# Performance work log

Hardware: AMD Instinct MI355X
Metric: run time of the kernel (lower is better)

Reference implementation:

```python
import jax, jax.numpy as jnp
import numpy as np

B, L, D, M, H = 32, 4096, 512, 64, 8
HD = D // H  # head dim = 64
NEG = -1e9


def setup_inputs() -> dict:
    key = jax.random.key(0)
    ks = jax.random.split(key, 12)
    s = 1.0 / np.sqrt(D)
    return {
        "query_features": jax.random.normal(ks[0], (B, L, D), jnp.float32),
        "mask": jax.random.randint(ks[1], (B, L), 0, 2, jnp.int32),
        "memory": jax.random.normal(ks[2], (M, D), jnp.float32),
        "Wq": jax.random.normal(ks[3], (D, D), jnp.float32) * s,
        "bq": jax.random.normal(ks[4], (D,), jnp.float32) * 0.01,
        "Wk": jax.random.normal(ks[5], (D, D), jnp.float32) * s,
        "bk": jax.random.normal(ks[6], (D,), jnp.float32) * 0.01,
        "Wv": jax.random.normal(ks[7], (D, D), jnp.float32) * s,
        "bv": jax.random.normal(ks[8], (D,), jnp.float32) * 0.01,
        "Wo": jax.random.normal(ks[9], (D, D), jnp.float32) * s,
        "bo": jax.random.normal(ks[10], (D,), jnp.float32) * 0.01,
    }


def reference(query_features, mask, memory, Wq, bq, Wk, bk, Wv, bv, Wo, bo):
    # read_memory: MHA(query=features, key=value=memory broadcast over batch)
    # with additive attn_mask of -1e9 on rows whose query position is invalid
    # (torch masks every key for an invalid query -> uniform attention there).
    q = (query_features @ Wq.T + bq).reshape(B, L, H, HD)
    k = (memory @ Wk.T + bk).reshape(M, H, HD)   # shared across batch
    v = (memory @ Wv.T + bv).reshape(M, H, HD)
    scores = jnp.einsum('blhd,mhd->bhlm', q, k) / np.sqrt(HD)  # [B,H,L,M]
    bias = jnp.where(mask[:, None, :, None] == 0, NEG, 0.0).astype(scores.dtype)
    attn = jax.nn.softmax(scores + bias, axis=-1)
    ctx = jnp.einsum('bhlm,mhd->blhd', attn, v).reshape(B, L, D)
    return ctx @ Wo.T + bo
```

## Files before the change

kernel.cpp:

```cpp
#include <hip/hip_runtime.h>
#include <hip/hip_bf16.h>

#define DD 512
#define HDIM 64
#define NROWS 131072

typedef __bf16 bf16x8 __attribute__((ext_vector_type(8)));
typedef float f32x4 __attribute__((ext_vector_type(4)));

static __device__ __forceinline__ unsigned bfbits(float f) {
    union { float f; unsigned u; } x; x.f = f;
    unsigned r = x.u + 0x7fffu + ((x.u >> 16) & 1u);
    return r >> 16;
}
static __device__ __forceinline__ __bf16 to_bf16(float f) {
    union { unsigned short s; __bf16 b; } y; y.s = (unsigned short)bfbits(f); return y.b;
}

static __device__ __forceinline__ int imgoff(int p, int g, int e) {
    return p * 64 + ((((g) ^ ((p) & 3) ^ (((p) >> 2) & 3)) & 3) << 4) + e * 2;
}

static __device__ __forceinline__ size_t fragoff(int c, int d) {
    return (size_t)((((c >> 6) * 64 + (d >> 5) * 4 + ((c >> 4) & 3)) << 10)
         + (((((d >> 3) & 3) << 4) + (c & 15)) << 4) + ((d & 7) << 1));
}

static __device__ __forceinline__ void gll16(const void* gsrc, void* ldst) {
    __builtin_amdgcn_global_load_lds(
        (const __attribute__((address_space(1))) unsigned int*)gsrc,
        (__attribute__((address_space(3))) unsigned int*)ldst, 16, 0, 0);
}

#define VMCNT(n) asm volatile("s_waitcnt vmcnt(" #n ")" ::: "memory")
#define LGKM0 asm volatile("s_waitcnt lgkmcnt(0)" ::: "memory")
#define MEMPIN asm volatile("" ::: "memory")

static __device__ __forceinline__ int xcd_swz(int bid, int nwg) {
    const int q = nwg >> 3, r = nwg & 7;
    const int xcd = bid & 7, idx = bid >> 3;
    return (xcd < r ? xcd * (q + 1) : r * (q + 1) + (xcd - r) * q) + idx;
}

__global__ void prep_kv(const float* __restrict__ memory,
                        const float* __restrict__ Wk, const float* __restrict__ bk,
                        const float* __restrict__ Wv, const float* __restrict__ bv,
                        float* __restrict__ kproj, float* __restrict__ vproj) {
    __shared__ float mrow[DD];
    const int m = blockIdx.x;
    const int t = threadIdx.x;
    for (int i = t; i < DD; i += 256) mrow[i] = memory[(size_t)m * DD + i];
    __syncthreads();
    for (int jj = 0; jj < 2; ++jj) {
        const int j = t + jj * 256;
        const float* wkr = Wk + (size_t)j * DD;
        const float* wvr = Wv + (size_t)j * DD;
        float sk = 0.f, sv = 0.f;
        for (int d = 0; d < DD; ++d) {
            const float md = mrow[d];
            sk += md * wkr[d];
            sv += md * wvr[d];
        }
        kproj[(size_t)m * DD + j] = sk + bk[j];
        vproj[(size_t)m * DD + j] = sv + bv[j];
    }
}

__global__ void prep_w(const float* __restrict__ Wq, const float* __restrict__ bq,
                       const float* __restrict__ Wo,
                       const float* __restrict__ kproj, const float* __restrict__ vproj,
                       char* __restrict__ W2img, float* __restrict__ b2,
                       char* __restrict__ W3fr) {
    const int i = blockIdx.x;
    const int t = threadIdx.x;
    __shared__ float kp[HDIM];
    __shared__ float worow[DD];
    const int m = i & 63, h = i >> 6;
    if (t < HDIM) kp[t] = kproj[(size_t)m * DD + h * HDIM + t];
    for (int d = t; d < DD; d += 256) worow[d] = Wo[(size_t)i * DD + d];
    __syncthreads();
    for (int dd2 = 0; dd2 < 2; ++dd2) {
        const int d = t + dd2 * 256;
        float s = 0.f;
        #pragma unroll 8
        for (int hd = 0; hd < HDIM; ++hd)
            s += Wq[(size_t)(h * HDIM + hd) * DD + d] * kp[hd];
        *(__bf16*)(W2img + (size_t)(d >> 5) * 32768 + imgoff(i, (d >> 3) & 3, d & 7)) = to_bf16(s);
    }
    if (t == 0) {
        float s = 0.f;
        for (int hd = 0; hd < HDIM; ++hd) s += bq[h * HDIM + hd] * kp[hd];
        b2[i] = s;
    }
    for (int cc = 0; cc < 2; ++cc) {
        const int c = t + cc * 256;
        const int mc = c & 63, hc = c >> 6;
        float s = 0.f;
        #pragma unroll 8
        for (int hd = 0; hd < HDIM; ++hd)
            s += vproj[(size_t)mc * DD + hc * HDIM + hd] * worow[hc * HDIM + hd];
        *(__bf16*)(W3fr + fragoff(i, c)) = to_bf16(s);
    }
}

__global__ __launch_bounds__(256, 2) void attn_fused(
    const float* __restrict__ x, const int* __restrict__ mask,
    const char* __restrict__ W2img, const float* __restrict__ b2,
    const char* __restrict__ W3fr, const float* __restrict__ bo,
    float* __restrict__ out) {
    __shared__ char ldsb[73728];

    const int tid = threadIdx.x;
    const int lane = tid & 63;
    const int wn = tid >> 6;
    const int lc = lane & 15, grp = lane >> 4;
    const int swz = xcd_swz(blockIdx.x, gridDim.x);
    const int gr0 = swz * 64;

    const int arow = tid >> 2, ag = tid & 3;
    const float* asrc = x + (size_t)(gr0 + arow) * DD + ag * 8;
    const int adst = imgoff(arow, ag, 0);
    const char* bsrc = W2img + wn * 8192 + lane * 16;

    f32x4 sreg[2][2];
    #define ALOAD(kt, set)                                                         \
        { sreg[set][0] = *(const f32x4*)(asrc + (kt) * 32);                        \
          sreg[set][1] = *(const f32x4*)(asrc + (kt) * 32 + 4); }
    #define AWRITE(buf, set)                                                       \
        { uint4 u;                                                                 \
          u.x = bfbits(sreg[set][0][0]) | (bfbits(sreg[set][0][1]) << 16);         \
          u.y = bfbits(sreg[set][0][2]) | (bfbits(sreg[set][0][3]) << 16);         \
          u.z = bfbits(sreg[set][1][0]) | (bfbits(sreg[set][1][1]) << 16);         \
          u.w = bfbits(sreg[set][1][2]) | (bfbits(sreg[set][1][3]) << 16);         \
          *(uint4*)(ldsb + (buf) * 4096 + adst) = u; }
    #define BGLL(kt, buf)                                                          \
        { _Pragma("unroll")                                                        \
          for (int g = 0; g < 8; ++g)                                              \
              gll16(bsrc + (size_t)(kt) * 32768 + g * 1024,                        \
                    ldsb + 8192 + (buf) * 32768 + wn * 8192 + g * 1024); }
    #define LDA1(buf, m)                                                           \
        (*(const bf16x8*)(ldsb + (buf) * 4096 + ((m) * 16 + lc) * 64               \
            + (((grp ^ (lc & 3) ^ (((m) * 4 + (lc >> 2)) & 3)) & 3) << 4)))
    #define LDB1(buf, n)                                                           \
        (*(const bf16x8*)(ldsb + 8192 + (buf) * 32768                              \
            + (wn * 128 + (n) * 16 + lc) * 64                                      \
            + (((grp ^ (lc & 3) ^ (((n) * 4 + (lc >> 2)) & 3)) & 3) << 4)))

    f32x4 acc[4][8];
    #pragma unroll
    for (int m = 0; m < 4; ++m)
        #pragma unroll
        for (int n = 0; n < 8; ++n) acc[m][n] = (f32x4){0.f, 0.f, 0.f, 0.f};

    BGLL(0, 0);
    MEMPIN;
    ALOAD(0, 0);
    MEMPIN;
    ALOAD(1, 1);
    VMCNT(2);
    AWRITE(0, 0);
    LGKM0;
    __builtin_amdgcn_s_barrier();
    __builtin_amdgcn_sched_barrier(0);

    #pragma unroll
    for (int s = 0; s < 16; ++s) {
        const int p = s & 1;
        if (s < 15) BGLL(s + 1, p ^ 1);
        MEMPIN;
        if (s < 14) ALOAD(s + 2, s & 1);
        bf16x8 af[4], bf[8];
        #pragma unroll
        for (int m = 0; m < 4; ++m) af[m] = LDA1(p, m);
        #pragma unroll
        for (int n = 0; n < 8; ++n) bf[n] = LDB1(p, n);
        __builtin_amdgcn_s_setprio(1);
        #pragma unroll
        for (int m = 0; m < 4; ++m)
            #pragma unroll
            for (int n = 0; n < 8; ++n)
                acc[m][n] = __builtin_amdgcn_mfma_f32_16x16x32_bf16(af[m], bf[n], acc[m][n], 0, 0, 0);
        __builtin_amdgcn_s_setprio(0);
        if (s < 14) {
            VMCNT(2);
            AWRITE(p ^ 1, (s + 1) & 1);
            LGKM0;
            __builtin_amdgcn_s_barrier();
            __builtin_amdgcn_sched_barrier(0);
        } else if (s < 15) {
            VMCNT(0);
            AWRITE(p ^ 1, 1);
            LGKM0;
            __builtin_amdgcn_s_barrier();
            __builtin_amdgcn_sched_barrier(0);
        }
    }
    __syncthreads();
    #undef ALOAD
    #undef AWRITE
    #undef BGLL
    #undef LDA1
    #undef LDB1

    const char* b3 = W3fr + wn * 131072 + lane * 16;
    #define LB3(kt, buf)                                                           \
        { _Pragma("unroll")                                                        \
          for (int n = 0; n < 8; ++n)                                              \
              bb3[buf][n] = *(const bf16x8*)(b3 + ((n) >> 2) * 65536               \
                  + (size_t)(kt) * 4096 + ((n) & 3) * 1024); }
    bf16x8 bb3[2][8];
    LB3(0, 0);

    float b2v[8];
    #pragma unroll
    for (int n = 0; n < 8; ++n) b2v[n] = b2[wn * 128 + n * 16 + lc];

    #pragma unroll
    for (int m = 0; m < 4; ++m) {
        const int4 mv = *(const int4*)(mask + gr0 + m * 16 + grp * 4);
        const int mk[4] = {mv.x, mv.y, mv.z, mv.w};
        #pragma unroll
        for (int hl = 0; hl < 2; ++hl) {
            #pragma unroll
            for (int j = 0; j < 4; ++j) {
                float s0 = (acc[m][hl * 4 + 0][j] + b2v[hl * 4 + 0]) * 0.125f;
                float s1 = (acc[m][hl * 4 + 1][j] + b2v[hl * 4 + 1]) * 0.125f;
                float s2 = (acc[m][hl * 4 + 2][j] + b2v[hl * 4 + 2]) * 0.125f;
                float s3 = (acc[m][hl * 4 + 3][j] + b2v[hl * 4 + 3]) * 0.125f;
                float mx = fmaxf(fmaxf(s0, s1), fmaxf(s2, s3));
                mx = fmaxf(mx, __shfl_xor(mx, 1));
                mx = fmaxf(mx, __shfl_xor(mx, 2));
                mx = fmaxf(mx, __shfl_xor(mx, 4));
                mx = fmaxf(mx, __shfl_xor(mx, 8));
                float p0 = __expf(s0 - mx);
                float p1 = __expf(s1 - mx);
                float p2 = __expf(s2 - mx);
                float p3 = __expf(s3 - mx);
                float sm = (p0 + p1) + (p2 + p3);
                sm += __shfl_xor(sm, 1);
                sm += __shfl_xor(sm, 2);
                sm += __shfl_xor(sm, 4);
                sm += __shfl_xor(sm, 8);
                float a[4];
                if (mk[j] == 0) {
                    a[0] = a[1] = a[2] = a[3] = 0.015625f;
                } else {
                    const float inv = 1.0f / sm;
                    a[0] = p0 * inv; a[1] = p1 * inv; a[2] = p2 * inv; a[3] = p3 * inv;
                }
                const int rl = m * 16 + grp * 4 + j;
                #pragma unroll
                for (int q = 0; q < 4; ++q) {
                    const int n = hl * 4 + q;
                    const int si = wn * 4 + (n >> 1);
                    const int g2 = (n & 1) * 2 + (lc >> 3);
                    const int off = 8192 + si * 4096 + rl * 64
                        + (((g2 ^ (rl & 3) ^ ((rl >> 2) & 3)) & 3) << 4)
                        + ((lc & 7) << 1);
                    *(short*)(ldsb + off) = (short)bfbits(a[q]);
                }
            }
        }
    }
    __syncthreads();

    #define LDA3(s, m)                                                             \
        (*(const bf16x8*)(ldsb + 8192 + (s) * 4096 + ((m) * 16 + lc) * 64          \
            + (((grp ^ (lc & 3) ^ (((m) * 4 + (lc >> 2)) & 3)) & 3) << 4)))

    #pragma unroll
    for (int m = 0; m < 4; ++m)
        #pragma unroll
        for (int n = 0; n < 8; ++n) acc[m][n] = (f32x4){0.f, 0.f, 0.f, 0.f};

    #pragma unroll
    for (int s = 0; s < 16; ++s) {
        const int p = s & 1;
        if (s < 15) LB3(s + 1, p ^ 1);
        bf16x8 af[4];
        #pragma unroll
        for (int m = 0; m < 4; ++m) af[m] = LDA3(s, m);
        __builtin_amdgcn_s_setprio(1);
        #pragma unroll
        for (int m = 0; m < 4; ++m)
            #pragma unroll
            for (int n = 0; n < 8; ++n)
                acc[m][n] = __builtin_amdgcn_mfma_f32_16x16x32_bf16(af[m], bb3[p][n], acc[m][n], 0, 0, 0);
        __builtin_amdgcn_s_setprio(0);
    }
    #undef LB3
    #undef LDA3

    float bov[8];
    #pragma unroll
    for (int n = 0; n < 8; ++n) bov[n] = bo[wn * 128 + n * 16 + lc];

    #pragma unroll
    for (int m = 0; m < 4; ++m) {
        #pragma unroll
        for (int j = 0; j < 4; ++j) {
            const int gr = gr0 + m * 16 + grp * 4 + j;
            float* orow = out + (size_t)gr * DD + wn * 128 + lc;
            #pragma unroll
            for (int n = 0; n < 8; ++n)
                __builtin_nontemporal_store(acc[m][n][j] + bov[n], orow + n * 16);
        }
    }
}

extern "C" void kernel_launch(void* const* d_in, const int* in_sizes, int n_in,
                              void* d_out, int out_size, void* d_ws, size_t ws_size,
                              hipStream_t stream) {
    const float* qf     = (const float*)d_in[0];
    const int*   mask   = (const int*)d_in[1];
    const float* memory = (const float*)d_in[2];
    const float* Wq     = (const float*)d_in[3];
    const float* bq     = (const float*)d_in[4];
    const float* Wk     = (const float*)d_in[5];
    const float* bk     = (const float*)d_in[6];
    const float* Wv     = (const float*)d_in[7];
    const float* bv     = (const float*)d_in[8];
    const float* Wo     = (const float*)d_in[9];
    const float* bo     = (const float*)d_in[10];

    char* ws = (char*)d_ws;
    float* kproj = (float*)ws;
    float* vproj = (float*)(ws + 131072);
    float* b2    = (float*)(ws + 262144);
    char*  W2img = ws + 264192;
    char*  W3fr  = ws + 788480;

    prep_kv<<<64, 256, 0, stream>>>(memory, Wk, bk, Wv, bv, kproj, vproj);
    prep_w<<<512, 256, 0, stream>>>(Wq, bq, Wo, kproj, vproj, W2img, b2, W3fr);
    attn_fused<<<NROWS / 64, 256, 0, stream>>>(qf, mask, W2img, b2, W3fr, bo, (float*)d_out);
}
```

Baseline: 267.3 us.

## Split 64-row tile across 16 waves in a 2x8 grid instead of 4

The fused attention block grows from 256 to 1024 threads, and each wave now owns a 32x64 output sub-tile (2 row groups by 8 column groups) instead of 64x128. Per-wave accumulator count drops fourfold, and global loads and LDS staging are split across the larger thread count. The aim is more waves in flight to hide memory latency and to cut register pressure. In exchange, each 64-row tile now needs more LDS fragment reads and W3 global loads, since A fragments are reread by 8 column waves, and barriers span 16 waves. LDS per block is unchanged at 72KB, which may cap how many blocks fit per CU.

```diff
diff --git a/kernel.cpp b/kernel.cpp
--- a/kernel.cpp
+++ b/kernel.cpp
@@ -7,6 +7,7 @@
 
 typedef __bf16 bf16x8 __attribute__((ext_vector_type(8)));
 typedef float f32x4 __attribute__((ext_vector_type(4)));
+typedef float f32x2 __attribute__((ext_vector_type(2)));
 
 static __device__ __forceinline__ unsigned bfbits(float f) {
     union { float f; unsigned u; } x; x.f = f;
@@ -103,7 +104,7 @@
     }
 }
 
-__global__ __launch_bounds__(256, 2) void attn_fused(
+__global__ __launch_bounds__(1024, 4) void attn_fused(
     const float* __restrict__ x, const int* __restrict__ mask,
     const char* __restrict__ W2img, const float* __restrict__ b2,
     const char* __restrict__ W3fr, const float* __restrict__ bo,
@@ -112,52 +113,48 @@
 
     const int tid = threadIdx.x;
     const int lane = tid & 63;
-    const int wn = tid >> 6;
+    const int wid = tid >> 6;
+    const int wr = wid >> 3;
+    const int wc = wid & 7;
     const int lc = lane & 15, grp = lane >> 4;
     const int swz = xcd_swz(blockIdx.x, gridDim.x);
     const int gr0 = swz * 64;
 
-    const int arow = tid >> 2, ag = tid & 3;
-    const float* asrc = x + (size_t)(gr0 + arow) * DD + ag * 8;
-    const int adst = imgoff(arow, ag, 0);
-    const char* bsrc = W2img + wn * 8192 + lane * 16;
-
-    f32x4 sreg[2][2];
-    #define ALOAD(kt, set)                                                         \
-        { sreg[set][0] = *(const f32x4*)(asrc + (kt) * 32);                        \
-          sreg[set][1] = *(const f32x4*)(asrc + (kt) * 32 + 4); }
+    const int arow = tid >> 4, sub = tid & 15;
+    const float* asrc = x + (size_t)(gr0 + arow) * DD + sub * 2;
+    const int adst = imgoff(arow, sub >> 2, (sub & 3) * 2);
+    const char* bsrc = W2img + wid * 2048 + lane * 16;
+
+    f32x2 sreg[2];
+    #define ALOAD(kt, set)  { sreg[set] = *(const f32x2*)(asrc + (kt) * 32); }
     #define AWRITE(buf, set)                                                       \
-        { uint4 u;                                                                 \
-          u.x = bfbits(sreg[set][0][0]) | (bfbits(sreg[set][0][1]) << 16);         \
-          u.y = bfbits(sreg[set][0][2]) | (bfbits(sreg[set][0][3]) << 16);         \
-          u.z = bfbits(sreg[set][1][0]) | (bfbits(sreg[set][1][1]) << 16);         \
-          u.w = bfbits(sreg[set][1][2]) | (bfbits(sreg[set][1][3]) << 16);         \
-          *(uint4*)(ldsb + (buf) * 4096 + adst) = u; }
+        { unsigned u = bfbits(sreg[set][0]) | (bfbits(sreg[set][1]) << 16);        \
+          *(unsigned*)(ldsb + (buf) * 4096 + adst) = u; }
     #define BGLL(kt, buf)                                                          \
-        { _Pragma("unroll")                                                        \
-          for (int g = 0; g < 8; ++g)                                              \
-              gll16(bsrc + (size_t)(kt) * 32768 + g * 1024,                        \
-                    ldsb + 8192 + (buf) * 32768 + wn * 8192 + g * 1024); }
+        { gll16(bsrc + (size_t)(kt) * 32768,                                       \
+                ldsb + 8192 + (buf) * 32768 + wid * 2048);                         \
+          gll16(bsrc + (size_t)(kt) * 32768 + 1024,                                \
+                ldsb + 8192 + (buf) * 32768 + wid * 2048 + 1024); }
     #define LDA1(buf, m)                                                           \
-        (*(const bf16x8*)(ldsb + (buf) * 4096 + ((m) * 16 + lc) * 64               \
+        (*(const bf16x8*)(ldsb + (buf) * 4096 + (wr * 32 + (m) * 16 + lc) * 64     \
             + (((grp ^ (lc & 3) ^ (((m) * 4 + (lc >> 2)) & 3)) & 3) << 4)))
     #define LDB1(buf, n)                                                           \
         (*(const bf16x8*)(ldsb + 8192 + (buf) * 32768                              \
-            + (wn * 128 + (n) * 16 + lc) * 64                                      \
+            + (wc * 64 + (n) * 16 + lc) * 64                                       \
             + (((grp ^ (lc & 3) ^ (((n) * 4 + (lc >> 2)) & 3)) & 3) << 4)))
 
-    f32x4 acc[4][8];
-    #pragma unroll
-    for (int m = 0; m < 4; ++m)
-        #pragma unroll
-        for (int n = 0; n < 8; ++n) acc[m][n] = (f32x4){0.f, 0.f, 0.f, 0.f};
+    f32x4 acc[2][4];
+    #pragma unroll
+    for (int m = 0; m < 2; ++m)
+        #pragma unroll
+        for (int n = 0; n < 4; ++n) acc[m][n] = (f32x4){0.f, 0.f, 0.f, 0.f};
 
     BGLL(0, 0);
     MEMPIN;
     ALOAD(0, 0);
     MEMPIN;
     ALOAD(1, 1);
-    VMCNT(2);
+    VMCNT(1);
     AWRITE(0, 0);
     LGKM0;
     __builtin_amdgcn_s_barrier();
@@ -169,20 +166,20 @@
         if (s < 15) BGLL(s + 1, p ^ 1);
         MEMPIN;
         if (s < 14) ALOAD(s + 2, s & 1);
-        bf16x8 af[4], bf[8];
-        #pragma unroll
-        for (int m = 0; m < 4; ++m) af[m] = LDA1(p, m);
-        #pragma unroll
-        for (int n = 0; n < 8; ++n) bf[n] = LDB1(p, n);
+        bf16x8 af[2], bf[4];
+        #pragma unroll
+        for (int m = 0; m < 2; ++m) af[m] = LDA1(p, m);
+        #pragma unroll
+        for (int n = 0; n < 4; ++n) bf[n] = LDB1(p, n);
         __builtin_amdgcn_s_setprio(1);
         #pragma unroll
-        for (int m = 0; m < 4; ++m)
+        for (int m = 0; m < 2; ++m)
             #pragma unroll
-            for (int n = 0; n < 8; ++n)
+            for (int n = 0; n < 4; ++n)
                 acc[m][n] = __builtin_amdgcn_mfma_f32_16x16x32_bf16(af[m], bf[n], acc[m][n], 0, 0, 0);
         __builtin_amdgcn_s_setprio(0);
         if (s < 14) {
-            VMCNT(2);
+            VMCNT(1);
             AWRITE(p ^ 1, (s + 1) & 1);
             LGKM0;
             __builtin_amdgcn_s_barrier();
@@ -202,107 +199,102 @@
     #undef LDA1
     #undef LDB1
 
-    const char* b3 = W3fr + wn * 131072 + lane * 16;
+    const char* b3 = W3fr + wc * 65536 + lane * 16;
     #define LB3(kt, buf)                                                           \
         { _Pragma("unroll")                                                        \
-          for (int n = 0; n < 8; ++n)                                              \
-              bb3[buf][n] = *(const bf16x8*)(b3 + ((n) >> 2) * 65536               \
-                  + (size_t)(kt) * 4096 + ((n) & 3) * 1024); }
-    bf16x8 bb3[2][8];
+          for (int n = 0; n < 4; ++n)                                              \
+              bb3[buf][n] = *(const bf16x8*)(b3 + ((kt) * 4 + (n)) * 1024); }
+    bf16x8 bb3[2][4];
     LB3(0, 0);
 
-    float b2v[8];
-    #pragma unroll
-    for (int n = 0; n < 8; ++n) b2v[n] = b2[wn * 128 + n * 16 + lc];
-
-    #pragma unroll
-    for (int m = 0; m < 4; ++m) {
-        const int4 mv = *(const int4*)(mask + gr0 + m * 16 + grp * 4);
+    float b2v[4];
+    #pragma unroll
+    for (int n = 0; n < 4; ++n) b2v[n] = b2[wc * 64 + n * 16 + lc];
+
+    #pragma unroll
+    for (int m = 0; m < 2; ++m) {
+        const int4 mv = *(const int4*)(mask + gr0 + wr * 32 + m * 16 + grp * 4);
         const int mk[4] = {mv.x, mv.y, mv.z, mv.w};
         #pragma unroll
-        for (int hl = 0; hl < 2; ++hl) {
+        for (int j = 0; j < 4; ++j) {
+            float s0 = (acc[m][0][j] + b2v[0]) * 0.125f;
+            float s1 = (acc[m][1][j] + b2v[1]) * 0.125f;
+            float s2 = (acc[m][2][j] + b2v[2]) * 0.125f;
+            float s3 = (acc[m][3][j] + b2v[3]) * 0.125f;
+            float mx = fmaxf(fmaxf(s0, s1), fmaxf(s2, s3));
+            mx = fmaxf(mx, __shfl_xor(mx, 1));
+            mx = fmaxf(mx, __shfl_xor(mx, 2));
+            mx = fmaxf(mx, __shfl_xor(mx, 4));
+            mx = fmaxf(mx, __shfl_xor(mx, 8));
+            float p0 = __expf(s0 - mx);
+            float p1 = __expf(s1 - mx);
+            float p2 = __expf(s2 - mx);
+            float p3 = __expf(s3 - mx);
+            float sm = (p0 + p1) + (p2 + p3);
+            sm += __shfl_xor(sm, 1);
+            sm += __shfl_xor(sm, 2);
+            sm += __shfl_xor(sm, 4);
+            sm += __shfl_xor(sm, 8);
+            float a[4];
+            if (mk[j] == 0) {
+                a[0] = a[1] = a[2] = a[3] = 0.015625f;
+            } else {
+                const float inv = 1.0f / sm;
+                a[0] = p0 * inv; a[1] = p1 * inv; a[2] = p2 * inv; a[3] = p3 * inv;
+            }
+            const int rl = wr * 32 + m * 16 + grp * 4 + j;
             #pragma unroll
-            for (int j = 0; j < 4; ++j) {
-                float s0 = (acc[m][hl * 4 + 0][j] + b2v[hl * 4 + 0]) * 0.125f;
-                float s1 = (acc[m][hl * 4 + 1][j] + b2v[hl * 4 + 1]) * 0.125f;
-                float s2 = (acc[m][hl * 4 + 2][j] + b2v[hl * 4 + 2]) * 0.125f;
-                float s3 = (acc[m][hl * 4 + 3][j] + b2v[hl * 4 + 3]) * 0.125f;
-                float mx = fmaxf(fmaxf(s0, s1), fmaxf(s2, s3));
-                mx = fmaxf(mx, __shfl_xor(mx, 1));
-                mx = fmaxf(mx, __shfl_xor(mx, 2));
-                mx = fmaxf(mx, __shfl_xor(mx, 4));
-                mx = fmaxf(mx, __shfl_xor(mx, 8));
-                float p0 = __expf(s0 - mx);
-                float p1 = __expf(s1 - mx);
-                float p2 = __expf(s2 - mx);
-                float p3 = __expf(s3 - mx);
-                float sm = (p0 + p1) + (p2 + p3);
-                sm += __shfl_xor(sm, 1);
-                sm += __shfl_xor(sm, 2);
-                sm += __shfl_xor(sm, 4);
-                sm += __shfl_xor(sm, 8);
-                float a[4];
-                if (mk[j] == 0) {
-                    a[0] = a[1] = a[2] = a[3] = 0.015625f;
-                } else {
-                    const float inv = 1.0f / sm;
-                    a[0] = p0 * inv; a[1] = p1 * inv; a[2] = p2 * inv; a[3] = p3 * inv;
-                }
-                const int rl = m * 16 + grp * 4 + j;
-                #pragma unroll
-                for (int q = 0; q < 4; ++q) {
-                    const int n = hl * 4 + q;
-                    const int si = wn * 4 + (n >> 1);
-                    const int g2 = (n & 1) * 2 + (lc >> 3);
-                    const int off = 8192 + si * 4096 + rl * 64
-                        + (((g2 ^ (rl & 3) ^ ((rl >> 2) & 3)) & 3) << 4)
-                        + ((lc & 7) << 1);
-                    *(short*)(ldsb + off) = (short)bfbits(a[q]);
-                }
+            for (int q = 0; q < 4; ++q) {
+                const int si = wc * 2 + (q >> 1);
+                const int g2 = (q & 1) * 2 + (lc >> 3);
+                const int off = 8192 + si * 4096 + rl * 64
+                    + (((g2 ^ (rl & 3) ^ ((rl >> 2) & 3)) & 3) << 4)
+                    + ((lc & 7) << 1);
+                *(short*)(ldsb + off) = (short)bfbits(a[q]);
             }
         }
     }
     __syncthreads();
 
     #define LDA3(s, m)                                                             \
-        (*(const bf16x8*)(ldsb + 8192 + (s) * 4096 + ((m) * 16 + lc) * 64          \
+        (*(const bf16x8*)(ldsb + 8192 + (s) * 4096 + (wr * 32 + (m) * 16 + lc) * 64 \
             + (((grp ^ (lc & 3) ^ (((m) * 4 + (lc >> 2)) & 3)) & 3) << 4)))
 
     #pragma unroll
-    for (int m = 0; m < 4; ++m)
-        #pragma unroll
-        for (int n = 0; n < 8; ++n) acc[m][n] = (f32x4){0.f, 0.f, 0.f, 0.f};
+    for (int m = 0; m < 2; ++m)
+        #pragma unroll
+        for (int n = 0; n < 4; ++n) acc[m][n] = (f32x4){0.f, 0.f, 0.f, 0.f};
 
     #pragma unroll
     for (int s = 0; s < 16; ++s) {
         const int p = s & 1;
         if (s < 15) LB3(s + 1, p ^ 1);
-        bf16x8 af[4];
-        #pragma unroll
-        for (int m = 0; m < 4; ++m) af[m] = LDA3(s, m);
+        bf16x8 af[2];
+        #pragma unroll
+        for (int m = 0; m < 2; ++m) af[m] = LDA3(s, m);
         __builtin_amdgcn_s_setprio(1);
         #pragma unroll
-        for (int m = 0; m < 4; ++m)
+        for (int m = 0; m < 2; ++m)
             #pragma unroll
-            for (int n = 0; n < 8; ++n)
+            for (int n = 0; n < 4; ++n)
                 acc[m][n] = __builtin_amdgcn_mfma_f32_16x16x32_bf16(af[m], bb3[p][n], acc[m][n], 0, 0, 0);
         __builtin_amdgcn_s_setprio(0);
     }
     #undef LB3
     #undef LDA3
 
-    float bov[8];
-    #pragma unroll
-    for (int n = 0; n < 8; ++n) bov[n] = bo[wn * 128 + n * 16 + lc];
-
-    #pragma unroll
-    for (int m = 0; m < 4; ++m) {
+    float bov[4];
+    #pragma unroll
+    for (int n = 0; n < 4; ++n) bov[n] = bo[wc * 64 + n * 16 + lc];
+
+    #pragma unroll
+    for (int m = 0; m < 2; ++m) {
         #pragma unroll
         for (int j = 0; j < 4; ++j) {
-            const int gr = gr0 + m * 16 + grp * 4 + j;
-            float* orow = out + (size_t)gr * DD + wn * 128 + lc;
+            const int gr = gr0 + wr * 32 + m * 16 + grp * 4 + j;
+            float* orow = out + (size_t)gr * DD + wc * 64 + lc;
             #pragma unroll
-            for (int n = 0; n < 8; ++n)
+            for (int n = 0; n < 4; ++n)
                 __builtin_nontemporal_store(acc[m][n][j] + bov[n], orow + n * 16);
         }
     }
@@ -332,5 +324,5 @@
 
     prep_kv<<<64, 256, 0, stream>>>(memory, Wk, bk, Wv, bv, kproj, vproj);
     prep_w<<<512, 256, 0, stream>>>(Wq, bq, Wo, kproj, vproj, W2img, b2, W3fr);
-    attn_fused<<<NROWS / 64, 256, 0, stream>>>(qf, mask, W2img, b2, W3fr, bo, (float*)d_out);
-}
+    attn_fused<<<NROWS / 64, 1024, 0, stream>>>(qf, mask, W2img, b2, W3fr, bo, (float*)d_out);
+}
```

Result: slower. 318.8 us (+19.3%).
